# Optimization experiments

Measured on AMD Instinct MI355X. Metric: run time of the kernel, lower is better.

The kernel has to match this reference:

```python
import jax, jax.numpy as jnp
import numpy as np

N_NODES = 100000
N_EDGES = 1600000
NFEAT, NHID, NCLASS = 128, 64, 40
DROPOUT_P = 0.5


def setup_inputs() -> dict:
    key = jax.random.key(0)
    k1, k2, k3, k4 = jax.random.split(key, 4)
    inputs = jax.random.normal(k1, (N_NODES, NFEAT), dtype=jnp.float32)
    edge_index = jax.random.randint(k2, (2, N_EDGES), 0, N_NODES, dtype=jnp.int64)
    # Glorot-uniform-ish init like torch Linear / PyG GCNConv
    lim1 = float(np.sqrt(6.0 / (NFEAT + NHID)))
    lim2 = float(np.sqrt(6.0 / (NHID + NCLASS)))
    W1 = jax.random.uniform(k3, (NFEAT, NHID), minval=-lim1, maxval=lim1, dtype=jnp.float32)
    W2 = jax.random.uniform(k4, (NHID, NCLASS), minval=-lim2, maxval=lim2, dtype=jnp.float32)
    b1 = jnp.zeros((NHID,), dtype=jnp.float32)
    b2 = jnp.zeros((NCLASS,), dtype=jnp.float32)
    return {"inputs": inputs, "edge_index": edge_index, "W1": W1, "b1": b1, "W2": W2, "b2": b2}


def _gcn_conv(x, W, b, src, dst, norm, n_nodes):
    # PyG GCNConv: out[i] = sum_{j->i} norm_ij * (x W)[j] + b
    xw = x @ W                              # [N, out_dim]
    msg = xw[src] * norm[:, None]           # [E+N, out_dim] gather + scale
    out = jax.ops.segment_sum(msg, dst, num_segments=n_nodes)  # scatter-add
    return out + b


def reference(inputs, edge_index, W1, b1, W2, b2):
    n = inputs.shape[0]
    loops = jnp.arange(n, dtype=edge_index.dtype)
    src = jnp.concatenate([edge_index[0], loops])   # add self-loops
    dst = jnp.concatenate([edge_index[1], loops])
    # symmetric normalization D^{-1/2} (A+I) D^{-1/2}
    deg = jax.ops.segment_sum(jnp.ones_like(src, dtype=inputs.dtype), dst, num_segments=n)
    dis = jnp.where(deg > 0, jax.lax.rsqrt(jnp.maximum(deg, 1.0)), 0.0)
    norm = dis[src] * dis[dst]
    # dropout on inputs (training mode, fixed key for determinism)
    keep = jax.random.bernoulli(jax.random.key(42), 1.0 - DROPOUT_P, inputs.shape)
    x = jnp.where(keep, inputs / (1.0 - DROPOUT_P), 0.0)
    h = jax.nn.relu(_gcn_conv(x, W1, b1, src, dst, norm, n))
    out = _gcn_conv(h, W2, b2, src, dst, norm, n)
    return out
```

## Files before the change

kernel.cpp:

```cpp
#include <hip/hip_runtime.h>

#define NF 128
#define NH 64
#define NC 40
#define BSHIFT 10
#define NB 98
#define BIN_T 8192
#define BSTRIDE 20480

typedef __attribute__((ext_vector_type(8))) short short8;
typedef __attribute__((ext_vector_type(4))) float float4v;

__device__ __forceinline__ unsigned rotl32(unsigned v, int s) { return (v << s) | (v >> (32 - s)); }

__device__ __forceinline__ unsigned short f2bf(float f) {
  unsigned u = __float_as_uint(f);
  return (unsigned short)((u + 0x7FFFu + ((u >> 16) & 1u)) >> 16);
}
__device__ __forceinline__ float bf2f(unsigned short b) {
  return __uint_as_float(((unsigned)b) << 16);
}

__device__ __forceinline__ unsigned threefry_bits(unsigned idx) {
  const unsigned k0 = 0u, k1 = 42u;
  const unsigned k2x = 0u ^ 42u ^ 0x1BD11BDAu;
  unsigned x0 = 0u, x1 = idx;
  x0 += k0; x1 += k1;
  x0 += x1; x1 = rotl32(x1, 13); x1 ^= x0;
  x0 += x1; x1 = rotl32(x1, 15); x1 ^= x0;
  x0 += x1; x1 = rotl32(x1, 26); x1 ^= x0;
  x0 += x1; x1 = rotl32(x1, 6);  x1 ^= x0;
  x0 += k1; x1 += k2x + 1u;
  x0 += x1; x1 = rotl32(x1, 17); x1 ^= x0;
  x0 += x1; x1 = rotl32(x1, 29); x1 ^= x0;
  x0 += x1; x1 = rotl32(x1, 16); x1 ^= x0;
  x0 += x1; x1 = rotl32(x1, 24); x1 ^= x0;
  x0 += k2x; x1 += k0 + 2u;
  x0 += x1; x1 = rotl32(x1, 13); x1 ^= x0;
  x0 += x1; x1 = rotl32(x1, 15); x1 ^= x0;
  x0 += x1; x1 = rotl32(x1, 26); x1 ^= x0;
  x0 += x1; x1 = rotl32(x1, 6);  x1 ^= x0;
  x0 += k0; x1 += k1 + 3u;
  x0 += x1; x1 = rotl32(x1, 17); x1 ^= x0;
  x0 += x1; x1 = rotl32(x1, 29); x1 ^= x0;
  x0 += x1; x1 = rotl32(x1, 16); x1 ^= x0;
  x0 += x1; x1 = rotl32(x1, 24); x1 ^= x0;
  x0 += k1; x1 += k2x + 4u;
  x0 += x1; x1 = rotl32(x1, 13); x1 ^= x0;
  x0 += x1; x1 = rotl32(x1, 15); x1 ^= x0;
  x0 += x1; x1 = rotl32(x1, 26); x1 ^= x0;
  x0 += x1; x1 = rotl32(x1, 6);  x1 ^= x0;
  x0 += k2x; x1 += k0 + 5u;
  return x0 ^ x1;
}

__global__ __launch_bounds__(256) void k_bin(const int* __restrict__ src, const int* __restrict__ dst,
                                             int* __restrict__ gcur, unsigned* __restrict__ binned,
                                             const float* __restrict__ W1, const float* __restrict__ W2,
                                             unsigned short* __restrict__ Wt1b, unsigned short* __restrict__ Wt2b,
                                             int nE, int nbin) {
  int t = threadIdx.x;
  if (blockIdx.x >= nbin) {
    int id = (blockIdx.x - nbin) * 256 + t;
    if (id < NF * NH) {
      int k = id >> 6, c = id & 63;
      Wt1b[c * NF + k] = f2bf(W1[id]);
    } else if (id < NF * NH + 48 * NH) {
      int id2 = id - NF * NH;
      int c = id2 >> 6, k = id2 & 63;
      Wt2b[c * NH + k] = (c < NC) ? f2bf(W2[k * NC + c]) : 0;
    }
    return;
  }
  __shared__ int h[NB];
  __shared__ int off[NB];
  int b0 = blockIdx.x * BIN_T;
  int b1 = b0 + BIN_T; if (b1 > nE) b1 = nE;
  if (t < NB) h[t] = 0;
  __syncthreads();
  for (int e = b0 + t; e < b1; e += 256)
    atomicAdd(&h[dst[e] >> BSHIFT], 1);
  __syncthreads();
  if (t < NB && h[t] > 0) off[t] = t * BSTRIDE + atomicAdd(&gcur[t], h[t]);
  __syncthreads();
  for (int e = b0 + t; e < b1; e += 256) {
    int s = src[e], d = dst[e];
    int p = atomicAdd(&off[d >> BSHIFT], 1);
    binned[p] = ((unsigned)s << BSHIFT) | (unsigned)(d & ((1 << BSHIFT) - 1));
  }
}

__global__ __launch_bounds__(1024) void k_fillb(const unsigned* __restrict__ binned, const int* __restrict__ gcur,
                                                unsigned* __restrict__ rpd, float* __restrict__ dis,
                                                int* __restrict__ csrc, int n) {
  __shared__ int hist[1024];
  __shared__ int wsum[16];
  int b = blockIdx.x;
  int base = b << BSHIFT;
  int t = threadIdx.x;
  int lo = b * BSTRIDE, hi = lo + gcur[b];
  hist[t] = 0;
  __syncthreads();
  for (int e = lo + t; e < hi; e += 1024)
    atomicAdd(&hist[binned[e] & 1023u], 1);
  __syncthreads();
  int v = hist[t];
  int sv = v;
#pragma unroll
  for (int off = 1; off < 64; off <<= 1) {
    int u = __shfl_up(sv, off);
    if ((t & 63) >= off) sv += u;
  }
  int wid = t >> 6;
  if ((t & 63) == 63) wsum[wid] = sv;
  __syncthreads();
  if (t < 16) {
    int ws = wsum[t];
    int sws = ws;
#pragma unroll
    for (int off = 1; off < 16; off <<= 1) {
      int u = __shfl_up(sws, off);
      if (t >= off) sws += u;
    }
    wsum[t] = sws - ws;
  }
  __syncthreads();
  int excl = sv - v + wsum[wid];
  if (base + t < n) {
    rpd[base + t] = ((unsigned)(lo + excl) << 11) | (unsigned)v;
    dis[base + t] = rsqrtf((float)(v + 1));
  }
  __syncthreads();
  hist[t] = lo + excl;
  __syncthreads();
  for (int e = lo + t; e < hi; e += 1024) {
    unsigned p = binned[e];
    int pos = atomicAdd(&hist[p & 1023u], 1);
    csrc[pos] = (int)(p >> BSHIFT);
  }
}

__global__ __launch_bounds__(256) void k_xw(const float* __restrict__ x, const unsigned short* __restrict__ Wt1b,
                                            const float* __restrict__ dis, unsigned short* __restrict__ y1b, int n) {
  __shared__ unsigned short Ws[NH * 136];
  __shared__ unsigned short xs[16 * 136];
  int t = threadIdx.x;
  int nodeBase = blockIdx.x * 16;
  for (int id = t; id < NH * 16; id += 256) {
    int c = id >> 4, kc = id & 15;
    *(short8*)&Ws[c * 136 + kc * 8] = *(const short8*)&Wt1b[c * NF + kc * 8];
  }
  {
    int nloc = t >> 4, kbase = (t & 15) * 8;
    int ebase = (nodeBase + nloc) * NF + kbase;
    const float4* xp = (const float4*)x;
    float4 a = xp[(ebase >> 2)];
    float4 b = xp[(ebase >> 2) + 1];
    float v[8] = {a.x, a.y, a.z, a.w, b.x, b.y, b.z, b.w};
#pragma unroll
    for (int q = 0; q < 8; ++q) {
      unsigned idx = (unsigned)(ebase + q);
      bool keep = (threefry_bits(idx) & 0x80000000u) == 0u;
      xs[nloc * 136 + kbase + q] = keep ? f2bf(v[q] * 2.0f) : 0;
    }
  }
  __syncthreads();
  int w = t >> 6, lane = t & 63;
  int m = lane & 15, quad = lane >> 4;
  float4v acc = {0.f, 0.f, 0.f, 0.f};
#pragma unroll
  for (int ks = 0; ks < 4; ++ks) {
    short8 a = *(const short8*)&xs[m * 136 + ks * 32 + quad * 8];
    short8 b = *(const short8*)&Ws[(w * 16 + m) * 136 + ks * 32 + quad * 8];
    acc = __builtin_amdgcn_mfma_f32_16x16x32_bf16(a, b, acc, 0, 0, 0);
  }
#pragma unroll
  for (int r = 0; r < 4; ++r) {
    int node = nodeBase + quad * 4 + r;
    y1b[node * NH + w * 16 + m] = f2bf(acc[r] * dis[node]);
  }
}

#define ACC8(u) \
  a0 += __uint_as_float((u).x << 16); \
  a1 += __uint_as_float((u).x & 0xFFFF0000u); \
  a2 += __uint_as_float((u).y << 16); \
  a3 += __uint_as_float((u).y & 0xFFFF0000u); \
  a4 += __uint_as_float((u).z << 16); \
  a5 += __uint_as_float((u).z & 0xFFFF0000u); \
  a6 += __uint_as_float((u).w << 16); \
  a7 += __uint_as_float((u).w & 0xFFFF0000u);

__device__ __forceinline__ unsigned packbf(float lo, float hi) {
  return (unsigned)f2bf(lo) | ((unsigned)f2bf(hi) << 16);
}

__global__ __launch_bounds__(256) void k_agg1(const unsigned short* __restrict__ y1b, const unsigned* __restrict__ rpd,
                                              const int* __restrict__ csrc, const float* __restrict__ dis,
                                              const float* __restrict__ b1, unsigned short* __restrict__ gb, int n) {
  int i = blockIdx.x * 32 + (threadIdx.x >> 3);
  if (i >= n) return;
  int fl = (threadIdx.x & 7) << 3;
  float di = dis[i];
  float4 bb0 = *(const float4*)&b1[fl];
  float4 bb1 = *(const float4*)&b1[fl + 4];
  const uint4 us = *(const uint4*)&y1b[(i << 6) + fl];
  float a0 = __uint_as_float(us.x << 16);
  float a1 = __uint_as_float(us.x & 0xFFFF0000u);
  float a2 = __uint_as_float(us.y << 16);
  float a3 = __uint_as_float(us.y & 0xFFFF0000u);
  float a4 = __uint_as_float(us.z << 16);
  float a5 = __uint_as_float(us.z & 0xFFFF0000u);
  float a6 = __uint_as_float(us.w << 16);
  float a7 = __uint_as_float(us.w & 0xFFFF0000u);
  unsigned rd = rpd[i];
  int lo = (int)(rd >> 11), hi = lo + (int)(rd & 2047u);
  int e = lo;
  int s0, s1, s2, s3;
  if (e + 4 <= hi) { s0 = csrc[e]; s1 = csrc[e + 1]; s2 = csrc[e + 2]; s3 = csrc[e + 3]; }
  for (; e + 8 <= hi; e += 4) {
    uint4 u0 = *(const uint4*)&y1b[(s0 << 6) + fl];
    uint4 u1 = *(const uint4*)&y1b[(s1 << 6) + fl];
    uint4 u2 = *(const uint4*)&y1b[(s2 << 6) + fl];
    uint4 u3 = *(const uint4*)&y1b[(s3 << 6) + fl];
    s0 = csrc[e + 4]; s1 = csrc[e + 5]; s2 = csrc[e + 6]; s3 = csrc[e + 7];
    ACC8(u0) ACC8(u1) ACC8(u2) ACC8(u3)
  }
  if (e + 4 <= hi) {
    uint4 u0 = *(const uint4*)&y1b[(s0 << 6) + fl];
    uint4 u1 = *(const uint4*)&y1b[(s1 << 6) + fl];
    uint4 u2 = *(const uint4*)&y1b[(s2 << 6) + fl];
    uint4 u3 = *(const uint4*)&y1b[(s3 << 6) + fl];
    ACC8(u0) ACC8(u1) ACC8(u2) ACC8(u3)
    e += 4;
  }
  for (; e < hi; ++e) {
    int s = csrc[e];
    uint4 u = *(const uint4*)&y1b[(s << 6) + fl];
    ACC8(u)
  }
  uint4 o;
  o.x = packbf(di * fmaxf(fmaf(di, a0, bb0.x), 0.f), di * fmaxf(fmaf(di, a1, bb0.y), 0.f));
  o.y = packbf(di * fmaxf(fmaf(di, a2, bb0.z), 0.f), di * fmaxf(fmaf(di, a3, bb0.w), 0.f));
  o.z = packbf(di * fmaxf(fmaf(di, a4, bb1.x), 0.f), di * fmaxf(fmaf(di, a5, bb1.y), 0.f));
  o.w = packbf(di * fmaxf(fmaf(di, a6, bb1.z), 0.f), di * fmaxf(fmaf(di, a7, bb1.w), 0.f));
  *(uint4*)&gb[(i << 6) + fl] = o;
}

__global__ __launch_bounds__(256) void k_agg2(const unsigned short* __restrict__ gb, const unsigned* __restrict__ rpd,
                                              const int* __restrict__ csrc, const float* __restrict__ dis,
                                              const unsigned short* __restrict__ Wt2b, const float* __restrict__ b2,
                                              float* __restrict__ out, int n) {
  __shared__ unsigned short Ws[48 * 72];
  __shared__ unsigned short ahs[32 * 72];
  int t = threadIdx.x;
  int nodeBase = blockIdx.x * 32;
  for (int id = t; id < 48 * 8; id += 256) {
    int c = id >> 3, kc = id & 7;
    *(short8*)&Ws[c * 72 + kc * 8] = *(const short8*)&Wt2b[c * NH + kc * 8];
  }
  int i = nodeBase + (t >> 3);
  int fl = (t & 7) << 3;
  if (i < n) {
    float di = dis[i];
    const uint4 us = *(const uint4*)&gb[(i << 6) + fl];
    float a0 = __uint_as_float(us.x << 16);
    float a1 = __uint_as_float(us.x & 0xFFFF0000u);
    float a2 = __uint_as_float(us.y << 16);
    float a3 = __uint_as_float(us.y & 0xFFFF0000u);
    float a4 = __uint_as_float(us.z << 16);
    float a5 = __uint_as_float(us.z & 0xFFFF0000u);
    float a6 = __uint_as_float(us.w << 16);
    float a7 = __uint_as_float(us.w & 0xFFFF0000u);
    unsigned rd = rpd[i];
    int lo = (int)(rd >> 11), hi = lo + (int)(rd & 2047u);
    int e = lo;
    int s0, s1, s2, s3;
    if (e + 4 <= hi) { s0 = csrc[e]; s1 = csrc[e + 1]; s2 = csrc[e + 2]; s3 = csrc[e + 3]; }
    for (; e + 8 <= hi; e += 4) {
      uint4 u0 = *(const uint4*)&gb[(s0 << 6) + fl];
      uint4 u1 = *(const uint4*)&gb[(s1 << 6) + fl];
      uint4 u2 = *(const uint4*)&gb[(s2 << 6) + fl];
      uint4 u3 = *(const uint4*)&gb[(s3 << 6) + fl];
      s0 = csrc[e + 4]; s1 = csrc[e + 5]; s2 = csrc[e + 6]; s3 = csrc[e + 7];
      ACC8(u0) ACC8(u1) ACC8(u2) ACC8(u3)
    }
    if (e + 4 <= hi) {
      uint4 u0 = *(const uint4*)&gb[(s0 << 6) + fl];
      uint4 u1 = *(const uint4*)&gb[(s1 << 6) + fl];
      uint4 u2 = *(const uint4*)&gb[(s2 << 6) + fl];
      uint4 u3 = *(const uint4*)&gb[(s3 << 6) + fl];
      ACC8(u0) ACC8(u1) ACC8(u2) ACC8(u3)
      e += 4;
    }
    for (; e < hi; ++e) {
      int s = csrc[e];
      uint4 u = *(const uint4*)&gb[(s << 6) + fl];
      ACC8(u)
    }
    uint4 o;
    o.x = packbf(di * a0, di * a1);
    o.y = packbf(di * a2, di * a3);
    o.z = packbf(di * a4, di * a5);
    o.w = packbf(di * a6, di * a7);
    *(uint4*)&ahs[(t >> 3) * 72 + fl] = o;
  }
  __syncthreads();
  int w = t >> 6, lane = t & 63;
  int m = lane & 15, quad = lane >> 4;
  if (w < 3) {
#pragma unroll
    for (int mt = 0; mt < 2; ++mt) {
      float4v acc = {0.f, 0.f, 0.f, 0.f};
#pragma unroll
      for (int ks = 0; ks < 2; ++ks) {
        short8 a = *(const short8*)&ahs[(mt * 16 + m) * 72 + ks * 32 + quad * 8];
        short8 b = *(const short8*)&Ws[(w * 16 + m) * 72 + ks * 32 + quad * 8];
        acc = __builtin_amdgcn_mfma_f32_16x16x32_bf16(a, b, acc, 0, 0, 0);
      }
      int col = w * 16 + m;
      if (col < NC) {
        float bias = b2[col];
#pragma unroll
        for (int r = 0; r < 4; ++r) {
          int node = nodeBase + mt * 16 + quad * 4 + r;
          if (node < n) out[node * NC + col] = acc[r] + bias;
        }
      }
    }
  }
}

extern "C" void kernel_launch(void* const* d_in, const int* in_sizes, int n_in,
                              void* d_out, int out_size, void* d_ws, size_t ws_size,
                              hipStream_t stream) {
  const float* x  = (const float*)d_in[0];
  const int*   ei = (const int*)d_in[1];
  const float* W1 = (const float*)d_in[2];
  const float* b1 = (const float*)d_in[3];
  const float* W2 = (const float*)d_in[4];
  const float* b2 = (const float*)d_in[5];
  float* out = (float*)d_out;
  int n  = in_sizes[0] / NF;
  int nE = in_sizes[1] / 2;
  const int* src = ei;
  const int* dst = ei + nE;

  char* ws = (char*)d_ws;
  float*    dis  = (float*)(ws + 0);
  unsigned* rpd  = (unsigned*)(ws + 400000);
  int*      gcur = (int*)(ws + 800000);
  unsigned short* Wt1b = (unsigned short*)(ws + 800512);
  unsigned short* Wt2b = (unsigned short*)(ws + 816896);
  int*      csrc = (int*)(ws + 823296);
  unsigned short* y1b = (unsigned short*)(ws + 8851456);
  unsigned short* gb  = (unsigned short*)(ws + 21651456);
  unsigned* binned = (unsigned*)(ws + 21651456);

  hipMemsetAsync(gcur, 0, NB * 4, stream);

  int nbin = (nE + BIN_T - 1) / BIN_T;
  int nprep = (NF * NH + 48 * NH + 255) / 256;
  k_bin  <<<nbin + nprep, 256, 0, stream>>>(src, dst, gcur, binned, W1, W2, Wt1b, Wt2b, nE, nbin);
  k_fillb<<<NB, 1024, 0, stream>>>(binned, gcur, rpd, dis, csrc, n);
  k_xw   <<<n / 16, 256, 0, stream>>>(x, Wt1b, dis, y1b, n);
  k_agg1 <<<(n + 31) / 32, 256, 0, stream>>>(y1b, rpd, csrc, dis, b1, gb, n);
  k_agg2 <<<(n + 31) / 32, 256, 0, stream>>>(gb, rpd, csrc, dis, Wt2b, b2, out, n);
}
```

Measured before the change: 223.6 us.

## Sort nodes by degree class to balance aggregation warps; shrink bin tile

```diff
diff --git a/kernel.cpp b/kernel.cpp
--- a/kernel.cpp
+++ b/kernel.cpp
@@ -5,7 +5,7 @@
 #define NC 40
 #define BSHIFT 10
 #define NB 98
-#define BIN_T 8192
+#define BIN_T 2048
 #define BSTRIDE 20480
 
 typedef __attribute__((ext_vector_type(8))) short short8;
@@ -92,14 +92,16 @@
 
 __global__ __launch_bounds__(1024) void k_fillb(const unsigned* __restrict__ binned, const int* __restrict__ gcur,
                                                 unsigned* __restrict__ rpd, float* __restrict__ dis,
-                                                int* __restrict__ csrc, int n) {
+                                                int* __restrict__ csrc, int* __restrict__ clscnt, int n) {
   __shared__ int hist[1024];
   __shared__ int wsum[16];
+  __shared__ int clsh[64];
   int b = blockIdx.x;
   int base = b << BSHIFT;
   int t = threadIdx.x;
   int lo = b * BSTRIDE, hi = lo + gcur[b];
   hist[t] = 0;
+  if (t < 64) clsh[t] = 0;
   __syncthreads();
   for (int e = lo + t; e < hi; e += 1024)
     atomicAdd(&hist[binned[e] & 1023u], 1);
@@ -129,8 +131,10 @@
   if (base + t < n) {
     rpd[base + t] = ((unsigned)(lo + excl) << 11) | (unsigned)v;
     dis[base + t] = rsqrtf((float)(v + 1));
-  }
-  __syncthreads();
+    atomicAdd(&clsh[v > 63 ? 63 : v], 1);
+  }
+  __syncthreads();
+  if (t < 64 && clsh[t]) atomicAdd(&clscnt[t], clsh[t]);
   hist[t] = lo + excl;
   __syncthreads();
   for (int e = lo + t; e < hi; e += 1024) {
@@ -141,10 +145,21 @@
 }
 
 __global__ __launch_bounds__(256) void k_xw(const float* __restrict__ x, const unsigned short* __restrict__ Wt1b,
-                                            const float* __restrict__ dis, unsigned short* __restrict__ y1b, int n) {
+                                            const float* __restrict__ dis, unsigned short* __restrict__ y1b,
+                                            const int* __restrict__ clscnt, int* __restrict__ clsbase, int n) {
   __shared__ unsigned short Ws[NH * 136];
   __shared__ unsigned short xs[16 * 136];
   int t = threadIdx.x;
+  if (blockIdx.x == 0 && t < 64) {
+    int c = clscnt[t];
+    int s = c;
+#pragma unroll
+    for (int off = 1; off < 64; off <<= 1) {
+      int u = __shfl_up(s, off);
+      if (t >= off) s += u;
+    }
+    clsbase[t] = s - c;
+  }
   int nodeBase = blockIdx.x * 16;
   for (int id = t; id < NH * 16; id += 256) {
     int c = id >> 4, kc = id & 15;
@@ -178,6 +193,17 @@
   for (int r = 0; r < 4; ++r) {
     int node = nodeBase + quad * 4 + r;
     y1b[node * NH + w * 16 + m] = f2bf(acc[r] * dis[node]);
+  }
+}
+
+__global__ __launch_bounds__(1024) void k_perm(const unsigned* __restrict__ rpd, const int* __restrict__ clsbase,
+                                               int* __restrict__ clscur, int* __restrict__ perm, int n) {
+  int i = blockIdx.x * 1024 + threadIdx.x;
+  if (i < n) {
+    int deg = (int)(rpd[i] & 2047u);
+    int cls = deg > 63 ? 63 : deg;
+    int pos = clsbase[cls] + atomicAdd(&clscur[cls], 1);
+    perm[pos] = i;
   }
 }
 
@@ -197,9 +223,11 @@
 
 __global__ __launch_bounds__(256) void k_agg1(const unsigned short* __restrict__ y1b, const unsigned* __restrict__ rpd,
                                               const int* __restrict__ csrc, const float* __restrict__ dis,
-                                              const float* __restrict__ b1, unsigned short* __restrict__ gb, int n) {
-  int i = blockIdx.x * 32 + (threadIdx.x >> 3);
-  if (i >= n) return;
+                                              const float* __restrict__ b1, const int* __restrict__ perm,
+                                              unsigned short* __restrict__ gb, int n) {
+  int slot = blockIdx.x * 32 + (threadIdx.x >> 3);
+  if (slot >= n) return;
+  int i = perm[slot];
   int fl = (threadIdx.x & 7) << 3;
   float di = dis[i];
   float4 bb0 = *(const float4*)&b1[fl];
@@ -250,18 +278,21 @@
 __global__ __launch_bounds__(256) void k_agg2(const unsigned short* __restrict__ gb, const unsigned* __restrict__ rpd,
                                               const int* __restrict__ csrc, const float* __restrict__ dis,
                                               const unsigned short* __restrict__ Wt2b, const float* __restrict__ b2,
-                                              float* __restrict__ out, int n) {
+                                              const int* __restrict__ perm, float* __restrict__ out, int n) {
   __shared__ unsigned short Ws[48 * 72];
   __shared__ unsigned short ahs[32 * 72];
+  __shared__ int pvt[32];
   int t = threadIdx.x;
-  int nodeBase = blockIdx.x * 32;
+  int slotBase = blockIdx.x * 32;
   for (int id = t; id < 48 * 8; id += 256) {
     int c = id >> 3, kc = id & 7;
     *(short8*)&Ws[c * 72 + kc * 8] = *(const short8*)&Wt2b[c * NH + kc * 8];
   }
-  int i = nodeBase + (t >> 3);
+  int slot = slotBase + (t >> 3);
   int fl = (t & 7) << 3;
-  if (i < n) {
+  if (slot < n) {
+    int i = perm[slot];
+    if ((t & 7) == 0) pvt[t >> 3] = i;
     float di = dis[i];
     const uint4 us = *(const uint4*)&gb[(i << 6) + fl];
     float a0 = __uint_as_float(us.x << 16);
@@ -323,8 +354,11 @@
         float bias = b2[col];
 #pragma unroll
         for (int r = 0; r < 4; ++r) {
-          int node = nodeBase + mt * 16 + quad * 4 + r;
-          if (node < n) out[node * NC + col] = acc[r] + bias;
+          int sl = mt * 16 + quad * 4 + r;
+          if (slotBase + sl < n) {
+            int node = pvt[sl];
+            out[node * NC + col] = acc[r] + bias;
+          }
         }
       }
     }
@@ -347,23 +381,28 @@
   const int* dst = ei + nE;
 
   char* ws = (char*)d_ws;
-  float*    dis  = (float*)(ws + 0);
-  unsigned* rpd  = (unsigned*)(ws + 400000);
-  int*      gcur = (int*)(ws + 800000);
-  unsigned short* Wt1b = (unsigned short*)(ws + 800512);
-  unsigned short* Wt2b = (unsigned short*)(ws + 816896);
-  int*      csrc = (int*)(ws + 823296);
-  unsigned short* y1b = (unsigned short*)(ws + 8851456);
-  unsigned short* gb  = (unsigned short*)(ws + 21651456);
-  unsigned* binned = (unsigned*)(ws + 21651456);
-
-  hipMemsetAsync(gcur, 0, NB * 4, stream);
+  float*    dis    = (float*)(ws + 0);
+  unsigned* rpd    = (unsigned*)(ws + 400000);
+  int*      gcur   = (int*)(ws + 800000);
+  int*      clscnt = (int*)(ws + 800392);
+  int*      clscur = (int*)(ws + 800648);
+  int*      clsbase= (int*)(ws + 800904);
+  unsigned short* Wt1b = (unsigned short*)(ws + 801280);
+  unsigned short* Wt2b = (unsigned short*)(ws + 817664);
+  int*      perm   = (int*)(ws + 823808);
+  int*      csrc   = (int*)(ws + 1223808);
+  unsigned short* y1b = (unsigned short*)(ws + 9251968);
+  unsigned short* gb  = (unsigned short*)(ws + 22051968);
+  unsigned* binned = (unsigned*)(ws + 22051968);
+
+  (void)hipMemsetAsync(gcur, 0, (NB + 128) * 4, stream);
 
   int nbin = (nE + BIN_T - 1) / BIN_T;
   int nprep = (NF * NH + 48 * NH + 255) / 256;
   k_bin  <<<nbin + nprep, 256, 0, stream>>>(src, dst, gcur, binned, W1, W2, Wt1b, Wt2b, nE, nbin);
-  k_fillb<<<NB, 1024, 0, stream>>>(binned, gcur, rpd, dis, csrc, n);
-  k_xw   <<<n / 16, 256, 0, stream>>>(x, Wt1b, dis, y1b, n);
-  k_agg1 <<<(n + 31) / 32, 256, 0, stream>>>(y1b, rpd, csrc, dis, b1, gb, n);
-  k_agg2 <<<(n + 31) / 32, 256, 0, stream>>>(gb, rpd, csrc, dis, Wt2b, b2, out, n);
-}
+  k_fillb<<<NB, 1024, 0, stream>>>(binned, gcur, rpd, dis, csrc, clscnt, n);
+  k_xw   <<<n / 16, 256, 0, stream>>>(x, Wt1b, dis, y1b, clscnt, clsbase, n);
+  k_perm <<<(n + 1023) / 1024, 1024, 0, stream>>>(rpd, clsbase, clscur, perm, n);
+  k_agg1 <<<(n + 31) / 32, 256, 0, stream>>>(y1b, rpd, csrc, dis, b1, perm, gb, n);
+  k_agg2 <<<(n + 31) / 32, 256, 0, stream>>>(gb, rpd, csrc, dis, Wt2b, b2, perm, out, n);
+}
```

Measured after the change: 519.9 us. +132.5%, slower.
